# Performance work log

Hardware: AMD Instinct MI355X
Metric: run time of the kernel (lower is better)

## Reference

```python
import jax, jax.numpy as jnp
import numpy as np


def fps_single(xyz, npoint):
    """Furthest point sampling. xyz: [N,3] -> [npoint] int32 indices (first = 0)."""
    d0 = jnp.sum((xyz - xyz[0]) ** 2, axis=-1)  # [N]

    def body(dists, _):
        nxt = jnp.argmax(dists)
        d = jnp.sum((xyz - xyz[nxt]) ** 2, axis=-1)
        return jnp.minimum(dists, d), nxt.astype(jnp.int32)

    _, idxs = jax.lax.scan(body, d0, None, length=npoint - 1)
    return jnp.concatenate([jnp.zeros((1,), jnp.int32), idxs])


def setup_inputs() -> dict:
    key = jax.random.key(0)
    k1, k2 = jax.random.split(key)
    B, N, C = 4, 8192, 128
    points = jax.random.normal(k1, (B, N, 3), dtype=jnp.float32)
    features = jax.random.normal(k2, (B, C, N), dtype=jnp.float32)
    return {"points": points, "features": features, "npoint": 2048, "nsample": 16}


def reference(points, features, npoint, nsample):
    """FPS downsample -> kNN grouping (mean pool) -> three_nn inverse-distance interpolation.
    points: [B,N,3], features: [B,C,N]. Returns interpolated features [B,C,N]."""
    B, N, _ = points.shape
    # --- furthest point sampling (Sample module) ---
    fps_idx = jax.vmap(lambda p: fps_single(p, npoint))(points)          # [B,Q]
    xyz_q = jnp.take_along_axis(points, fps_idx[..., None], axis=1)      # [B,Q,3]
    # --- pairwise squared distances query->all (pdist2squared) ---
    sq = (jnp.sum(xyz_q ** 2, -1)[:, :, None]
          + jnp.sum(points ** 2, -1)[:, None, :]
          - 2.0 * jnp.einsum('bqd,bnd->bqn', xyz_q, points))             # [B,Q,N]
    sq = jnp.maximum(sq, 0.0)
    # --- kNN neighbors, drop self (SampleNeighbors, knn=True takes topk nsample+1 then [:,:,1:]) ---
    _, nbr = jax.lax.top_k(-sq, nsample + 1)                             # [B,Q,K+1]
    nbr = nbr[..., 1:]                                                   # [B,Q,K]
    grouped = jax.vmap(lambda f, idx: f[:, idx])(features, nbr)          # [B,C,Q,K]
    coarse = jnp.mean(grouped, axis=-1)                                  # [B,C,Q]
    # --- three_nn + inverse squared-distance interpolation (GraphFPModule) ---
    neg_d3, i3 = jax.lax.top_k(-jnp.swapaxes(sq, 1, 2), 3)               # [B,N,3]
    d3 = jnp.maximum(-neg_d3, 1e-10)                                     # squared dists, clamped
    inv = 1.0 / (d3 + 1e-8)
    w = inv / jnp.sum(inv, axis=-1, keepdims=True)                       # [B,N,3]
    f3 = jax.vmap(lambda f, idx: f[:, idx])(coarse, i3)                  # [B,C,N,3]
    out = jnp.sum(f3 * w[:, None, :, :], axis=-1)                        # [B,C,N]
    return out
```

## Files before the change

### kernel.cpp

```cpp
#include <hip/hip_runtime.h>
#include <cstdint>
#include <cstddef>

#define Bq   4
#define Nq   8192
#define Cq   128
#define NPq  2048
#define KSEL 17

typedef float v2f __attribute__((ext_vector_type(2)));

__device__ __forceinline__ float rn_sq3(float x, float y, float z) {
  return __fadd_rn(__fadd_rn(__fmul_rn(x, x), __fmul_rn(y, y)), __fmul_rn(z, z));
}

__device__ __forceinline__ v2f dist2_v2(v2f px, v2f py, v2f pz, float cx, float cy, float cz) {
#pragma clang fp contract(off)
  v2f dx = px - cx;
  v2f dy = py - cy;
  v2f dz = pz - cz;
  v2f s = dx * dx + dy * dy + dz * dz;
  return s;
}

__device__ __forceinline__ float sq_expand(float qx, float qy, float qz, float sq_,
                                           float px, float py, float pz, float sp_) {
  float dot = __fadd_rn(__fadd_rn(__fmul_rn(qx, px), __fmul_rn(qy, py)), __fmul_rn(qz, pz));
  float v = __fsub_rn(__fadd_rn(sq_, sp_), __fmul_rn(2.0f, dot));
  v = fmaxf(v, 0.0f);
  return __fadd_rn(v, 0.0f);
}

__global__ __launch_bounds__(256) void k_sump(const float* __restrict__ pts,
                                              float* __restrict__ sump,
                                              float4* __restrict__ pxyzs) {
  int g = blockIdx.x * 256 + threadIdx.x;
  float x = pts[g * 3 + 0], y = pts[g * 3 + 1], z = pts[g * 3 + 2];
  float s = rn_sq3(x, y, z);
  sump[g] = s;
  pxyzs[g] = make_float4(x, y, z, s);
}

template <int CTRL, int RM, int BM>
__device__ __forceinline__ float dpp_maxf(float v) {
  int r = __builtin_amdgcn_update_dpp(__float_as_int(v), __float_as_int(v), CTRL, RM, BM, false);
  return fmaxf(v, __int_as_float(r));
}

__global__ __launch_bounds__(512) void k_fps(const float* __restrict__ pts,
                                             int* __restrict__ fps_idx) {
  const int b = blockIdx.x;
  const int tid = threadIdx.x;
  const int lane = tid & 63, wid = tid >> 6;
  const float* P = pts + (size_t)b * Nq * 3;

  __shared__ float sv[2][8];
  __shared__ int spi[2][8];
  __shared__ int idx_lds[NPq];

  v2f px[8], py[8], pz[8], dd[8];
  const int pbase = tid * 16;
#pragma unroll
  for (int j = 0; j < 8; j++) {
    const float2* q2 = (const float2*)(P + (size_t)(pbase + 2 * j) * 3);
    float2 A = q2[0], Bv = q2[1], Cv = q2[2];
    v2f tx, ty, tz;
    tx.x = A.x;  tx.y = Bv.y;
    ty.x = A.y;  ty.y = Cv.x;
    tz.x = Bv.x; tz.y = Cv.y;
    px[j] = tx; py[j] = ty; pz[j] = tz;
  }
  float qx = P[0], qy = P[1], qz = P[2];
  float bd = -1.0f;
  int bp = pbase;
#pragma unroll
  for (int j = 0; j < 8; j++) {
    v2f s = dist2_v2(px[j], py[j], pz[j], qx, qy, qz);
    dd[j] = s;
    if (s.x > bd) { bd = s.x; bp = pbase + 2 * j; }
    if (s.y > bd) { bd = s.y; bp = pbase + 2 * j + 1; }
  }
  if (tid == 0) idx_lds[0] = 0;

  for (int i = 1; i < NPq; i++) {
    float wv = bd;
    wv = dpp_maxf<0x111, 0xf, 0xf>(wv);
    wv = dpp_maxf<0x112, 0xf, 0xf>(wv);
    wv = dpp_maxf<0x114, 0xf, 0xf>(wv);
    wv = dpp_maxf<0x118, 0xf, 0xf>(wv);
    wv = dpp_maxf<0x142, 0xa, 0xf>(wv);
    wv = dpp_maxf<0x143, 0xc, 0xf>(wv);
    float wmax = __int_as_float(__builtin_amdgcn_readlane(__float_as_int(wv), 63));
    unsigned long long msk = __ballot(bd == wmax);
    int wl = (int)__ffsll(msk) - 1;
    int wbp = __shfl(bp, wl);
    if (lane == 0) { sv[i & 1][wid] = wmax; spi[i & 1][wid] = wbp; }
    __syncthreads();

    float bv = sv[i & 1][0];
    int bip = spi[i & 1][0];
#pragma unroll
    for (int w = 1; w < 8; w++) {
      float tv = sv[i & 1][w];
      bool t = tv > bv;
      bv = t ? tv : bv;
      bip = t ? spi[i & 1][w] : bip;
    }
    if (tid == 0) idx_lds[i] = bip;

    const float* cp = P + 3u * (unsigned int)bip;
    float cx = cp[0], cy = cp[1], cz = cp[2];

    bd = -1.0f;
    bp = pbase;
#pragma unroll
    for (int j = 0; j < 8; j++) {
      v2f s = dist2_v2(px[j], py[j], pz[j], cx, cy, cz);
      v2f nd;
      nd.x = fminf(dd[j].x, s.x);
      nd.y = fminf(dd[j].y, s.y);
      dd[j] = nd;
      if (nd.x > bd) { bd = nd.x; bp = pbase + 2 * j; }
      if (nd.y > bd) { bd = nd.y; bp = pbase + 2 * j + 1; }
    }
  }
  __syncthreads();
#pragma unroll
  for (int t = 0; t < NPq / 512; t++) {
    int g = t * 512 + tid;
    fps_idx[b * NPq + g] = idx_lds[g];
  }
}

__global__ __launch_bounds__(256) void k_gatherq(const float* __restrict__ pts,
                                                 const float* __restrict__ sump,
                                                 const int* __restrict__ fps_idx,
                                                 float* __restrict__ xyzq,
                                                 float* __restrict__ sumq,
                                                 float* __restrict__ xqs,
                                                 float* __restrict__ yqs,
                                                 float* __restrict__ zqs) {
  int g = blockIdx.x * 256 + threadIdx.x;
  int b = g >> 11;
  int idx = fps_idx[g];
  int src = b * Nq + idx;
  float x = pts[src * 3 + 0], y = pts[src * 3 + 1], z = pts[src * 3 + 2];
  xyzq[g * 3 + 0] = x;
  xyzq[g * 3 + 1] = y;
  xyzq[g * 3 + 2] = z;
  xqs[g] = x; yqs[g] = y; zqs[g] = z;
  sumq[g] = sump[src];
}

__global__ __launch_bounds__(256) void k_knn_group(const float4* __restrict__ pxyzs,
                                                   const float* __restrict__ xyzq,
                                                   const float* __restrict__ sumq,
                                                   const float* __restrict__ feats,
                                                   float* __restrict__ coarse_t) {
  const int blk = blockIdx.x;
  const int b = blk >> 11;
  const int tid = threadIdx.x;
  const int lane = tid & 63, wid = tid >> 6;
  const float4* PS = pxyzs + (size_t)b * Nq;

  __shared__ float sq_lds[Nq];
  __shared__ unsigned long long wk[2][4];
  __shared__ int sel[KSEL];

  float qx = xyzq[blk * 3 + 0], qy = xyzq[blk * 3 + 1], qz = xyzq[blk * 3 + 2];
  float sq_ = sumq[blk];

  unsigned long long lmin = ~0ull;
#pragma unroll
  for (int k = 0; k < 32; k++) {
    int p = k * 256 + tid;
    float4 t = PS[p];
    float v = sq_expand(qx, qy, qz, sq_, t.x, t.y, t.z, t.w);
    sq_lds[p] = v;
    unsigned long long key = ((unsigned long long)__float_as_uint(v) << 32) | (unsigned int)p;
    lmin = key < lmin ? key : lmin;
  }

  for (int r = 0; r < KSEL; r++) {
    unsigned long long key = lmin;
#pragma unroll
    for (int off = 32; off > 0; off >>= 1) {
      unsigned long long o = __shfl_down(key, off);
      key = o < key ? o : key;
    }
    if (lane == 0) wk[r & 1][wid] = key;
    __syncthreads();
    unsigned long long m = wk[r & 1][0];
    m = wk[r & 1][1] < m ? wk[r & 1][1] : m;
    m = wk[r & 1][2] < m ? wk[r & 1][2] : m;
    m = wk[r & 1][3] < m ? wk[r & 1][3] : m;
    int p = (int)(unsigned int)(m & 0xFFFFFFFFull);
    if (tid == 0) sel[r] = p;
    if ((p & 255) == tid) {
      sq_lds[p] = __uint_as_float(0x7f800000u);
      lmin = ~0ull;
#pragma unroll
      for (int k = 0; k < 32; k++) {
        int pp = k * 256 + tid;
        unsigned long long kk =
            ((unsigned long long)__float_as_uint(sq_lds[pp]) << 32) | (unsigned int)pp;
        lmin = kk < lmin ? kk : lmin;
      }
    }
  }
  __syncthreads();

  if (tid < Cq) {
    const float* F = feats + ((size_t)(b * Cq + tid)) * Nq;
    float acc = 0.0f;
#pragma unroll
    for (int j = 1; j < KSEL; j++) acc += F[sel[j]];
    coarse_t[(size_t)blk * Cq + tid] = acc * (1.0f / 16.0f);
  }
}

__device__ __forceinline__ void merge3(unsigned long long& a0, unsigned long long& a1,
                                       unsigned long long& a2, unsigned long long b0,
                                       unsigned long long b1, unsigned long long b2) {
  unsigned long long lo1 = a0 < b0 ? a0 : b0;
  unsigned long long hi1 = a0 < b0 ? b0 : a0;
  unsigned long long lo2 = a1 < b1 ? a1 : b1;
  unsigned long long hi2 = a1 < b1 ? b1 : a1;
  unsigned long long lo3 = a2 < b2 ? a2 : b2;
  unsigned long long c1 = hi1 < lo2 ? hi1 : lo2;
  unsigned long long m1 = hi1 < lo2 ? lo2 : hi1;
  unsigned long long m2 = hi2 < lo3 ? hi2 : lo3;
  a0 = lo1;
  a1 = c1;
  a2 = m1 < m2 ? m1 : m2;
}

__global__ __launch_bounds__(256) void k_three(const float* __restrict__ pts,
                                               const float* __restrict__ sump,
                                               const float* __restrict__ xqs,
                                               const float* __restrict__ yqs,
                                               const float* __restrict__ zqs,
                                               const float* __restrict__ sumq,
                                               int* __restrict__ i0, int* __restrict__ i1,
                                               int* __restrict__ i2, float* __restrict__ w0,
                                               float* __restrict__ w1, float* __restrict__ w2) {
  const int wid = threadIdx.x >> 6, lane = threadIdx.x & 63;
  const int n = blockIdx.x * 4 + wid;
  const int b = n >> 13;
  float px = pts[n * 3 + 0], py = pts[n * 3 + 1], pz = pts[n * 3 + 2];
  float sp = sump[n];
  const float* QX = xqs + (size_t)b * NPq;
  const float* QY = yqs + (size_t)b * NPq;
  const float* QZ = zqs + (size_t)b * NPq;
  const float* SQ = sumq + (size_t)b * NPq;

  unsigned long long k0 = ~0ull, k1 = ~0ull, k2 = ~0ull;
#pragma unroll 4
  for (int j = 0; j < 32; j++) {
    int q = lane + j * 64;
    float v = sq_expand(QX[q], QY[q], QZ[q], SQ[q], px, py, pz, sp);
    unsigned long long key = ((unsigned long long)__float_as_uint(v) << 32) | (unsigned int)q;
    if (key < k2) {
      if (key < k1) {
        k2 = k1;
        if (key < k0) { k1 = k0; k0 = key; } else { k1 = key; }
      } else {
        k2 = key;
      }
    }
  }
#pragma unroll
  for (int off = 32; off > 0; off >>= 1) {
    unsigned long long o0 = __shfl_down(k0, off);
    unsigned long long o1 = __shfl_down(k1, off);
    unsigned long long o2 = __shfl_down(k2, off);
    merge3(k0, k1, k2, o0, o1, o2);
  }
  if (lane == 0) {
    float v0 = __uint_as_float((unsigned int)(k0 >> 32));
    float v1 = __uint_as_float((unsigned int)(k1 >> 32));
    float v2 = __uint_as_float((unsigned int)(k2 >> 32));
    float d0 = fmaxf(v0, 1e-10f), d1 = fmaxf(v1, 1e-10f), d2 = fmaxf(v2, 1e-10f);
    float inv0 = 1.0f / (d0 + 1e-8f);
    float inv1 = 1.0f / (d1 + 1e-8f);
    float inv2 = 1.0f / (d2 + 1e-8f);
    float s = inv0 + inv1 + inv2;
    i0[n] = (int)(unsigned int)(k0 & 0xFFFFFFFFull);
    i1[n] = (int)(unsigned int)(k1 & 0xFFFFFFFFull);
    i2[n] = (int)(unsigned int)(k2 & 0xFFFFFFFFull);
    w0[n] = inv0 / s;
    w1[n] = inv1 / s;
    w2[n] = inv2 / s;
  }
}

__global__ __launch_bounds__(256) void k_interp(const float* __restrict__ coarse_t,
                                                const int* __restrict__ i0,
                                                const int* __restrict__ i1,
                                                const int* __restrict__ i2,
                                                const float* __restrict__ w0,
                                                const float* __restrict__ w1,
                                                const float* __restrict__ w2,
                                                float* __restrict__ out) {
  int g = blockIdx.x * 256 + threadIdx.x;
  int b = g >> 13, n = g & (Nq - 1);
  int a0 = i0[g], a1 = i1[g], a2 = i2[g];
  float u0 = w0[g], u1 = w1[g], u2 = w2[g];
  const float4* r0 = (const float4*)(coarse_t + ((size_t)b * NPq + a0) * Cq);
  const float4* r1 = (const float4*)(coarse_t + ((size_t)b * NPq + a1) * Cq);
  const float4* r2 = (const float4*)(coarse_t + ((size_t)b * NPq + a2) * Cq);
  float* O = out + (size_t)b * Cq * Nq + n;
#pragma unroll 4
  for (int cq = 0; cq < Cq / 4; cq++) {
    float4 f0 = r0[cq], f1 = r1[cq], f2 = r2[cq];
    float o0 = u0 * f0.x + u1 * f1.x + u2 * f2.x;
    float o1 = u0 * f0.y + u1 * f1.y + u2 * f2.y;
    float o2 = u0 * f0.z + u1 * f1.z + u2 * f2.z;
    float o3 = u0 * f0.w + u1 * f1.w + u2 * f2.w;
    O[(size_t)(cq * 4 + 0) * Nq] = o0;
    O[(size_t)(cq * 4 + 1) * Nq] = o1;
    O[(size_t)(cq * 4 + 2) * Nq] = o2;
    O[(size_t)(cq * 4 + 3) * Nq] = o3;
  }
}

extern "C" void kernel_launch(void* const* d_in, const int* in_sizes, int n_in,
                              void* d_out, int out_size, void* d_ws, size_t ws_size,
                              hipStream_t stream) {
  const float* pts = (const float*)d_in[0];
  const float* feats = (const float*)d_in[1];
  float* out = (float*)d_out;

  char* ws = (char*)d_ws;
  size_t off = 0;
  auto alloc = [&](size_t bytes) {
    void* p = ws + off;
    off += (bytes + 255) & ~(size_t)255;
    return p;
  };
  float* sump = (float*)alloc((size_t)Bq * Nq * 4);
  float4* pxyzs = (float4*)alloc((size_t)Bq * Nq * 16);
  int* fps_idx = (int*)alloc((size_t)Bq * NPq * 4);
  float* xyzq = (float*)alloc((size_t)Bq * NPq * 3 * 4);
  float* sumq = (float*)alloc((size_t)Bq * NPq * 4);
  float* coarse_t = (float*)alloc((size_t)Bq * NPq * Cq * 4);
  int* i0 = (int*)alloc((size_t)Bq * Nq * 4);
  int* i1 = (int*)alloc((size_t)Bq * Nq * 4);
  int* i2 = (int*)alloc((size_t)Bq * Nq * 4);
  float* w0 = (float*)alloc((size_t)Bq * Nq * 4);
  float* w1 = (float*)alloc((size_t)Bq * Nq * 4);
  float* w2 = (float*)alloc((size_t)Bq * Nq * 4);
  float* xqs = (float*)alloc((size_t)Bq * NPq * 4);
  float* yqs = (float*)alloc((size_t)Bq * NPq * 4);
  float* zqs = (float*)alloc((size_t)Bq * NPq * 4);

  k_sump<<<(Bq * Nq) / 256, 256, 0, stream>>>(pts, sump, pxyzs);
  k_fps<<<Bq, 512, 0, stream>>>(pts, fps_idx);
  k_gatherq<<<(Bq * NPq) / 256, 256, 0, stream>>>(pts, sump, fps_idx, xyzq, sumq, xqs, yqs, zqs);
  k_knn_group<<<Bq * NPq, 256, 0, stream>>>(pxyzs, xyzq, sumq, feats, coarse_t);
  k_three<<<(Bq * Nq) / 4, 256, 0, stream>>>(pts, sump, xqs, yqs, zqs, sumq, i0, i1, i2, w0, w1, w2);
  k_interp<<<(Bq * Nq) / 256, 256, 0, stream>>>(coarse_t, i0, i1, i2, w0, w1, w2, out);
}
```

Measured before the change: 2.396 ms.

## Spatially sort points and skip FPS distance updates via bounding-box pruning

A new kernel buckets each batch's points into a coarse 8x8x8 Morton grid so that every FPS thread owns a spatially compact set of 16 points, storing the original index alongside the coordinates. FPS then keeps a per-thread bounding box and skips the min-distance update for a whole wavefront when no lane's box can be closer to the new centroid than that lane's current max distance. Argmax ties are broken on the original index with a DPP min-reduction, preserving first-index semantics. This adds a sort kernel and extra per-iteration reduction work on the serial FPS loop, and the pruning payoff depends on how much of the data the bounding boxes let each wavefront skip.

```diff
diff --git a/kernel.cpp b/kernel.cpp
--- a/kernel.cpp
+++ b/kernel.cpp
@@ -41,44 +41,114 @@
   pxyzs[g] = make_float4(x, y, z, s);
 }
 
+__device__ __forceinline__ int morton9(float x, float y, float z) {
+  int qx = (int)fminf(fmaxf((x + 5.0f) * 0.8f, 0.0f), 7.0f);
+  int qy = (int)fminf(fmaxf((y + 5.0f) * 0.8f, 0.0f), 7.0f);
+  int qz = (int)fminf(fmaxf((z + 5.0f) * 0.8f, 0.0f), 7.0f);
+  int m = 0;
+#pragma unroll
+  for (int bit = 0; bit < 3; bit++) {
+    m |= ((qx >> bit) & 1) << (3 * bit + 2);
+    m |= ((qy >> bit) & 1) << (3 * bit + 1);
+    m |= ((qz >> bit) & 1) << (3 * bit + 0);
+  }
+  return m;
+}
+
+__global__ __launch_bounds__(512) void k_sort(const float* __restrict__ pts,
+                                              float4* __restrict__ sorted4) {
+  const int b = blockIdx.x, tid = threadIdx.x;
+  const float* P = pts + (size_t)b * Nq * 3;
+  __shared__ int hist[512];
+  __shared__ int offs[512];
+  hist[tid] = 0;
+  __syncthreads();
+  float xs[16], ys[16], zs[16];
+  int cl[16];
+#pragma unroll
+  for (int k = 0; k < 16; k++) {
+    int p = tid * 16 + k;
+    xs[k] = P[p * 3 + 0];
+    ys[k] = P[p * 3 + 1];
+    zs[k] = P[p * 3 + 2];
+    cl[k] = morton9(xs[k], ys[k], zs[k]);
+    atomicAdd(&hist[cl[k]], 1);
+  }
+  __syncthreads();
+  if (tid < 64) {
+    int base[8], s = 0;
+#pragma unroll
+    for (int j = 0; j < 8; j++) { base[j] = s; s += hist[tid * 8 + j]; }
+    int v = s;
+#pragma unroll
+    for (int o = 1; o < 64; o <<= 1) {
+      int t = __shfl_up(v, o);
+      if (tid >= o) v += t;
+    }
+    int excl = v - s;
+#pragma unroll
+    for (int j = 0; j < 8; j++) offs[tid * 8 + j] = excl + base[j];
+  }
+  __syncthreads();
+  float4* S = sorted4 + (size_t)b * Nq;
+#pragma unroll
+  for (int k = 0; k < 16; k++) {
+    int pos = atomicAdd(&offs[cl[k]], 1);
+    S[pos] = make_float4(xs[k], ys[k], zs[k], __int_as_float(tid * 16 + k));
+  }
+}
+
 template <int CTRL, int RM, int BM>
 __device__ __forceinline__ float dpp_maxf(float v) {
   int r = __builtin_amdgcn_update_dpp(__float_as_int(v), __float_as_int(v), CTRL, RM, BM, false);
   return fmaxf(v, __int_as_float(r));
 }
+template <int CTRL, int RM, int BM>
+__device__ __forceinline__ unsigned dpp_minu(unsigned v) {
+  int r = __builtin_amdgcn_update_dpp((int)v, (int)v, CTRL, RM, BM, false);
+  unsigned u = (unsigned)r;
+  return u < v ? u : v;
+}
 
 __global__ __launch_bounds__(512) void k_fps(const float* __restrict__ pts,
+                                             const float4* __restrict__ sorted4,
                                              int* __restrict__ fps_idx) {
-  const int b = blockIdx.x;
-  const int tid = threadIdx.x;
+  const int b = blockIdx.x, tid = threadIdx.x;
   const int lane = tid & 63, wid = tid >> 6;
   const float* P = pts + (size_t)b * Nq * 3;
+  const float4* S = sorted4 + (size_t)b * Nq;
 
   __shared__ float sv[2][8];
   __shared__ int spi[2][8];
   __shared__ int idx_lds[NPq];
 
   v2f px[8], py[8], pz[8], dd[8];
+  int og[16];
   const int pbase = tid * 16;
+  float blx = 1e30f, bly = 1e30f, blz = 1e30f;
+  float bhx = -1e30f, bhy = -1e30f, bhz = -1e30f;
 #pragma unroll
   for (int j = 0; j < 8; j++) {
-    const float2* q2 = (const float2*)(P + (size_t)(pbase + 2 * j) * 3);
-    float2 A = q2[0], Bv = q2[1], Cv = q2[2];
+    float4 a = S[pbase + 2 * j];
+    float4 c = S[pbase + 2 * j + 1];
     v2f tx, ty, tz;
-    tx.x = A.x;  tx.y = Bv.y;
-    ty.x = A.y;  ty.y = Cv.x;
-    tz.x = Bv.x; tz.y = Cv.y;
+    tx.x = a.x; tx.y = c.x;
+    ty.x = a.y; ty.y = c.y;
+    tz.x = a.z; tz.y = c.z;
     px[j] = tx; py[j] = ty; pz[j] = tz;
+    og[2 * j] = __float_as_int(a.w);
+    og[2 * j + 1] = __float_as_int(c.w);
+    blx = fminf(blx, fminf(a.x, c.x)); bhx = fmaxf(bhx, fmaxf(a.x, c.x));
+    bly = fminf(bly, fminf(a.y, c.y)); bhy = fmaxf(bhy, fmaxf(a.y, c.y));
+    blz = fminf(blz, fminf(a.z, c.z)); bhz = fmaxf(bhz, fmaxf(a.z, c.z));
   }
   float qx = P[0], qy = P[1], qz = P[2];
   float bd = -1.0f;
-  int bp = pbase;
 #pragma unroll
   for (int j = 0; j < 8; j++) {
     v2f s = dist2_v2(px[j], py[j], pz[j], qx, qy, qz);
     dd[j] = s;
-    if (s.x > bd) { bd = s.x; bp = pbase + 2 * j; }
-    if (s.y > bd) { bd = s.y; bp = pbase + 2 * j + 1; }
+    bd = fmaxf(bd, fmaxf(s.x, s.y));
   }
   if (tid == 0) idx_lds[0] = 0;
 
@@ -91,10 +161,23 @@
     wv = dpp_maxf<0x142, 0xa, 0xf>(wv);
     wv = dpp_maxf<0x143, 0xc, 0xf>(wv);
     float wmax = __int_as_float(__builtin_amdgcn_readlane(__float_as_int(wv), 63));
-    unsigned long long msk = __ballot(bd == wmax);
-    int wl = (int)__ffsll(msk) - 1;
-    int wbp = __shfl(bp, wl);
-    if (lane == 0) { sv[i & 1][wid] = wmax; spi[i & 1][wid] = wbp; }
+    unsigned cand = 0xFFFFFFFFu;
+    if (bd == wmax) {
+#pragma unroll
+      for (int j = 0; j < 8; j++) {
+        if (dd[j].x == wmax) { unsigned o = (unsigned)og[2 * j];     cand = o < cand ? o : cand; }
+        if (dd[j].y == wmax) { unsigned o = (unsigned)og[2 * j + 1]; cand = o < cand ? o : cand; }
+      }
+    }
+    unsigned cm = cand;
+    cm = dpp_minu<0x111, 0xf, 0xf>(cm);
+    cm = dpp_minu<0x112, 0xf, 0xf>(cm);
+    cm = dpp_minu<0x114, 0xf, 0xf>(cm);
+    cm = dpp_minu<0x118, 0xf, 0xf>(cm);
+    cm = dpp_minu<0x142, 0xa, 0xf>(cm);
+    cm = dpp_minu<0x143, 0xc, 0xf>(cm);
+    unsigned worig = (unsigned)__builtin_amdgcn_readlane((int)cm, 63);
+    if (lane == 0) { sv[i & 1][wid] = wmax; spi[i & 1][wid] = (int)worig; }
     __syncthreads();
 
     float bv = sv[i & 1][0];
@@ -102,26 +185,32 @@
 #pragma unroll
     for (int w = 1; w < 8; w++) {
       float tv = sv[i & 1][w];
-      bool t = tv > bv;
+      int ti = spi[i & 1][w];
+      bool t = (tv > bv) || (tv == bv && ti < bip);
       bv = t ? tv : bv;
-      bip = t ? spi[i & 1][w] : bip;
+      bip = t ? ti : bip;
     }
     if (tid == 0) idx_lds[i] = bip;
 
-    const float* cp = P + 3u * (unsigned int)bip;
+    const float* cp = P + 3u * (unsigned)bip;
     float cx = cp[0], cy = cp[1], cz = cp[2];
 
-    bd = -1.0f;
-    bp = pbase;
-#pragma unroll
-    for (int j = 0; j < 8; j++) {
-      v2f s = dist2_v2(px[j], py[j], pz[j], cx, cy, cz);
-      v2f nd;
-      nd.x = fminf(dd[j].x, s.x);
-      nd.y = fminf(dd[j].y, s.y);
-      dd[j] = nd;
-      if (nd.x > bd) { bd = nd.x; bp = pbase + 2 * j; }
-      if (nd.y > bd) { bd = nd.y; bp = pbase + 2 * j + 1; }
+    float ex = fmaxf(fmaxf(blx - cx, cx - bhx), 0.0f);
+    float ey = fmaxf(fmaxf(bly - cy, cy - bhy), 0.0f);
+    float ez = fmaxf(fmaxf(blz - cz, cz - bhz), 0.0f);
+    float dmin2 = ex * ex + ey * ey + ez * ez;
+    bool act = dmin2 * 0.99999f < bd;
+    if (__ballot(act) != 0ull) {
+      bd = -1.0f;
+#pragma unroll
+      for (int j = 0; j < 8; j++) {
+        v2f s = dist2_v2(px[j], py[j], pz[j], cx, cy, cz);
+        v2f nd;
+        nd.x = fminf(dd[j].x, s.x);
+        nd.y = fminf(dd[j].y, s.y);
+        dd[j] = nd;
+        bd = fmaxf(bd, fmaxf(nd.x, nd.y));
+      }
     }
   }
   __syncthreads();
@@ -340,6 +429,7 @@
   };
   float* sump = (float*)alloc((size_t)Bq * Nq * 4);
   float4* pxyzs = (float4*)alloc((size_t)Bq * Nq * 16);
+  float4* sorted4 = (float4*)alloc((size_t)Bq * Nq * 16);
   int* fps_idx = (int*)alloc((size_t)Bq * NPq * 4);
   float* xyzq = (float*)alloc((size_t)Bq * NPq * 3 * 4);
   float* sumq = (float*)alloc((size_t)Bq * NPq * 4);
@@ -355,7 +445,8 @@
   float* zqs = (float*)alloc((size_t)Bq * NPq * 4);
 
   k_sump<<<(Bq * Nq) / 256, 256, 0, stream>>>(pts, sump, pxyzs);
-  k_fps<<<Bq, 512, 0, stream>>>(pts, fps_idx);
+  k_sort<<<Bq, 512, 0, stream>>>(pts, sorted4);
+  k_fps<<<Bq, 512, 0, stream>>>(pts, sorted4, fps_idx);
   k_gatherq<<<(Bq * NPq) / 256, 256, 0, stream>>>(pts, sump, fps_idx, xyzq, sumq, xqs, yqs, zqs);
   k_knn_group<<<Bq * NPq, 256, 0, stream>>>(pxyzs, xyzq, sumq, feats, coarse_t);
   k_three<<<(Bq * Nq) / 4, 256, 0, stream>>>(pts, sump, xqs, yqs, zqs, sumq, i0, i1, i2, w0, w1, w2);
```

Result: slower. 3.134 ms (+30.8%).
